# Kernel tuning notes

Hardware: AMD Instinct MI355X
Metric: run time of the kernel (lower is better)

## Reference

```python
import jax, jax.numpy as jnp
import numpy as np

NUM_TOKENS_SCORE = 64
NUM_HEADS = 16
NUM_KV_HEADS = 4
HEAD_SIZE = 128
SCALE = 0.08838834764831845  # 1/sqrt(128)


def setup_inputs() -> dict:
    key = jax.random.key(0)
    k1, k2, k3 = jax.random.split(key, 3)
    B, S = 2, 2048
    total = B * S
    return {
        "query": jax.random.normal(k1, (total, NUM_HEADS * HEAD_SIZE), dtype=jnp.float32),
        "key": jax.random.normal(k2, (total, NUM_KV_HEADS * HEAD_SIZE), dtype=jnp.float32),
        "value": jax.random.normal(k3, (total, NUM_KV_HEADS * HEAD_SIZE), dtype=jnp.float32),
        "batch_size": B,
        "seq_len": S,
    }


def reference(query, key, value, batch_size, seq_len):
    """Prompt-phase SparsePagedAttention: varlen causal GQA attention (equal
    prompt lengths -> dense [B,S] layout) plus the fused softmax score-sum over
    the last NUM_TOKENS_SCORE query rows used for KV-cache pruning."""
    B, S = batch_size, seq_len
    H, Hk, D = NUM_HEADS, NUM_KV_HEADS, HEAD_SIZE
    rep = H // Hk  # queries per kv head (head_mapping via repeat_interleave)

    q = query.reshape(B, S, H, D)
    k = jnp.repeat(key.reshape(B, S, Hk, D), rep, axis=2)    # [B,S,H,D]
    v = jnp.repeat(value.reshape(B, S, Hk, D), rep, axis=2)  # [B,S,H,D]

    scores = jnp.einsum('bqhd,bkhd->bhqk', q, k) * SCALE      # [B,H,S,S]
    causal = jnp.tril(jnp.ones((S, S), dtype=bool))
    scores = jnp.where(causal[None, None], scores, jnp.finfo(scores.dtype).min)
    probs = jax.nn.softmax(scores, axis=-1)                   # [B,H,S,S]

    out = jnp.einsum('bhqk,bkhd->bqhd', probs, v).reshape(B * S, H * D)
    # triton_fused_softmax_sum: sum softmax probs over last NUM_TOKENS_SCORE queries
    score_sum = probs[:, :, S - NUM_TOKENS_SCORE:, :].sum(axis=2)  # [B,H,S]
    return out, score_sum
```

## Files before the change

### kernel.cpp

```cpp
#include <hip/hip_runtime.h>


#define BB 2
#define SS 2048
#define NH 16
#define NKV 4
#define DD 128
#define TILE_SH 4096

typedef __attribute__((ext_vector_type(8))) short bf16x8;
typedef __attribute__((ext_vector_type(4))) float f32x4;

constexpr float SCL = 0.08838834764831845f * 1.4426950408889634f;

__device__ __forceinline__ short f2bf(float f) {
  union { float f; unsigned u; } v; v.f = f;
  unsigned r = v.u + 0x7FFFu + ((v.u >> 16) & 1u);
  return (short)(r >> 16);
}

__device__ __forceinline__ unsigned pack2bf(float a, float b) {
  union { float f; unsigned u; } x, y; x.f = a; y.f = b;
  return __builtin_amdgcn_perm(y.u, x.u, 0x07060302);
}

__device__ __forceinline__ void gl_lds16(const void* g, void* l) {
  __builtin_amdgcn_global_load_lds(
      (const __attribute__((address_space(1))) unsigned*)g,
      (__attribute__((address_space(3))) unsigned*)l, 16, 0, 0);
}

__global__ void prep(const float* __restrict__ K, const float* __restrict__ V,
                     short* __restrict__ Kb, short* __restrict__ Vb) {
  const int p = blockIdx.x;
  const int b = p >> 8, hk = (p >> 6) & 3, kt = p & 63;
  const int tid = threadIdx.x;
  const int k0 = kt * 32;
  short* kb = Kb + ((size_t)((b * 4 + hk) * 64 + kt)) * TILE_SH;
  short* vb = Vb + ((size_t)((b * 4 + hk) * 64 + kt)) * TILE_SH;
  {
    const int k = tid & 31, chb = tid >> 5;
    const float* src = K + ((size_t)(b * SS + k0 + k) * NKV + hk) * DD;
#pragma unroll
    for (int i = 0; i < 2; ++i) {
      const int ch = chb + i * 8;
      const float* s = src + ch * 8;
      float4 f0 = *(const float4*)s;
      float4 f1 = *(const float4*)(s + 4);
      bf16x8 t;
      t[0] = f2bf(f0.x); t[1] = f2bf(f0.y); t[2] = f2bf(f0.z); t[3] = f2bf(f0.w);
      t[4] = f2bf(f1.x); t[5] = f2bf(f1.y); t[6] = f2bf(f1.z); t[7] = f2bf(f1.w);
      *(bf16x8*)(kb + (ch * 32 + k) * 8) = t;
    }
  }
  {
    const int d = tid & 127, kcb = tid >> 7;
#pragma unroll
    for (int i = 0; i < 2; ++i) {
      const int kc = kcb + i * 2;
      const float* s = V + ((size_t)(b * SS + k0 + kc * 8) * NKV + hk) * DD + d;
      bf16x8 t;
#pragma unroll
      for (int e = 0; e < 8; ++e) t[e] = f2bf(s[(size_t)e * (NKV * DD)]);
      *(bf16x8*)(vb + (kc * 128 + d) * 8) = t;
    }
  }
}

__constant__ unsigned char RK2SLOT[48] = {
    15, 46, 47, 44, 45, 14, 42, 43, 40, 41, 13, 38, 39, 36, 37, 12,
    34, 35, 32, 33, 11, 30, 31, 28, 29, 10, 26, 27, 24, 25, 9,  22,
    23, 20, 21, 8,  18, 19, 16, 17, 7,  6,  5,  4,  3,  2,  1,  0};

__global__ __launch_bounds__(256, 4) void fa2(
    const float* __restrict__ Q, const short* __restrict__ Kb,
    const short* __restrict__ Vb, float* __restrict__ Out,
    float* __restrict__ Ob, float* __restrict__ l0a, float* __restrict__ l1a,
    float* __restrict__ wsl, const int mode) {
  __shared__ bf16x8 kv[2][1024];
  __shared__ short ldsP[4][640];

  const int tid = threadIdx.x;
  const int w = tid >> 6, lane = tid & 63;
  const int c = lane & 15, qd = lane >> 4;

  int qt, kb0, nit, part, bh;
  if (mode) {
    bh = blockIdx.x & 31;
    const int rank = blockIdx.x >> 5;
    const int slot = RK2SLOT[rank];
    if (slot < 16) {
      qt = slot; kb0 = 0; nit = 2 * qt + 2; part = 0;
    } else {
      const int s = slot - 16;
      qt = 16 + (s >> 1);
      if (s & 1) { kb0 = qt + 1; nit = qt + 1; part = 2; }
      else       { kb0 = 0;      nit = qt + 1; part = 1; }
    }
  } else {
    const int i = blockIdx.x;
    const int g = i >> 8, cc = i & 255;
    bh = cc >> 3;
    const int jp = cc & 7;
    qt = (g == 0) ? jp : (g == 1) ? 31 - jp : (g == 2) ? 8 + jp : 23 - jp;
    kb0 = 0; nit = 2 * qt + 2; part = 0;
  }
  const int b = bh >> 4, h = bh & 15, hk = h >> 2;

  const char* KT = (const char*)(Kb + ((size_t)(b * 4 + hk)) * 64 * TILE_SH);
  const char* VT = (const char*)(Vb + ((size_t)(b * 4 + hk)) * 64 * TILE_SH);

  auto stage = [&](int kt, int bi) {
    const char* sk = KT + (size_t)kt * 8192 + w * 2048 + lane * 16;
    const char* sv = VT + (size_t)kt * 8192 + w * 2048 + lane * 16;
    char* dk = (char*)kv[bi] + w * 2048;
    char* dv = dk + 8192;
#pragma unroll
    for (int t = 0; t < 2; ++t) {
      gl_lds16(sk + t * 1024, dk + t * 1024);
      gl_lds16(sv + t * 1024, dv + t * 1024);
    }
  };

  stage(kb0, 0);

  const float* qrow = Q + ((size_t)(b * SS + qt * 64 + w * 16 + c) * NH + h) * DD;
  bf16x8 qf[4];
#pragma unroll
  for (int ks = 0; ks < 4; ++ks) {
    const float* p = qrow + ks * 32 + qd * 8;
    float4 f0 = *(const float4*)p;
    float4 f1 = *(const float4*)(p + 4);
    bf16x8 t;
    t[0] = f2bf(f0.x * SCL); t[1] = f2bf(f0.y * SCL);
    t[2] = f2bf(f0.z * SCL); t[3] = f2bf(f0.w * SCL);
    t[4] = f2bf(f1.x * SCL); t[5] = f2bf(f1.y * SCL);
    t[6] = f2bf(f1.z * SCL); t[7] = f2bf(f1.w * SCL);
    qf[ks] = t;
  }

  f32x4 o[8];
#pragma unroll
  for (int dt = 0; dt < 8; ++dt) { o[dt][0] = 0.f; o[dt][1] = 0.f; o[dt][2] = 0.f; o[dt][3] = 0.f; }
  float l_part = 0.f;

  for (int it = 0; it < nit; ++it) {
    const int kt = kb0 + it;
    __syncthreads();
    const int cb = it & 1;
    if (it + 1 < nit) stage(kt + 1, cb ^ 1);

    const bf16x8* bK = kv[cb];
    const bf16x8* bV = kv[cb] + 512;

    f32x4 st0 = {0.f, 0.f, 0.f, 0.f}, st1 = {0.f, 0.f, 0.f, 0.f};
#pragma unroll
    for (int ks = 0; ks < 4; ++ks) {
      const int chz = (ks * 4 + qd) * 32;
      bf16x8 a0 = bK[chz + c];
      bf16x8 a1 = bK[chz + 16 + c];
      st0 = __builtin_amdgcn_mfma_f32_16x16x32_bf16(a0, qf[ks], st0, 0, 0, 0);
      st1 = __builtin_amdgcn_mfma_f32_16x16x32_bf16(a1, qf[ks], st1, 0, 0, 0);
    }

    float pr[8];
#pragma unroll
    for (int r = 0; r < 4; ++r) { pr[r] = exp2f(st0[r]); pr[4 + r] = exp2f(st1[r]); }
    const int koff = kt * 32 - qt * 64;
    if (koff >= 0) {
      const int qrl = w * 16 + c;
#pragma unroll
      for (int mt = 0; mt < 2; ++mt)
#pragma unroll
        for (int r = 0; r < 4; ++r)
          if (koff + mt * 16 + qd * 4 + r > qrl) pr[mt * 4 + r] = 0.f;
    }
#pragma unroll
    for (int x = 0; x < 8; ++x) l_part += pr[x];

    short* pp = ldsP[w] + c * 40;
#pragma unroll
    for (int mt = 0; mt < 2; ++mt) {
      union { short4 s4; unsigned u[2]; } pk;
      pk.u[0] = pack2bf(pr[mt * 4 + 0], pr[mt * 4 + 1]);
      pk.u[1] = pack2bf(pr[mt * 4 + 2], pr[mt * 4 + 3]);
      *(short4*)(pp + mt * 16 + qd * 4) = pk.s4;
    }
    __asm__ volatile("s_waitcnt lgkmcnt(0)" ::: "memory");
    bf16x8 pf = *(const bf16x8*)(pp + qd * 8);

#pragma unroll
    for (int dt = 0; dt < 8; ++dt)
      o[dt] = __builtin_amdgcn_mfma_f32_16x16x32_bf16(bV[qd * 128 + dt * 16 + c],
                                                      pf, o[dt], 0, 0, 0);
  }

  float l = l_part;
  l += __shfl_xor(l, 16);
  l += __shfl_xor(l, 32);

  if (part == 0) {
    const float linv = 1.f / l;
    float* orow = Out + ((size_t)(b * SS + qt * 64 + w * 16 + c) * NH + h) * DD;
#pragma unroll
    for (int dt = 0; dt < 8; ++dt) {
      float4 ov;
      ov.x = o[dt][0] * linv; ov.y = o[dt][1] * linv;
      ov.z = o[dt][2] * linv; ov.w = o[dt][3] * linv;
      *(float4*)(orow + dt * 16 + qd * 4) = ov;
    }
    if (!mode && qt == 31 && qd == 0)
      wsl[bh * 64 + w * 16 + c] = l;
  } else {
    const int qoff = (qt - 16) * 64 + w * 16 + c;
    float* dst = (part == 1)
        ? Out + ((size_t)(b * SS + qt * 64 + w * 16 + c) * NH + h) * DD
        : Ob + ((size_t)(bh * 1024 + qoff)) * DD;
#pragma unroll
    for (int dt = 0; dt < 8; ++dt)
      *(f32x4*)(dst + dt * 16 + qd * 4) = o[dt];
    if (qd == 0) {
      float* la = (part == 1) ? l0a : l1a;
      la[bh * 1024 + qoff] = l;
    }
  }
}

__global__ __launch_bounds__(256) void combine(
    float* __restrict__ Out, const float* __restrict__ Ob,
    const float* __restrict__ l0a, const float* __restrict__ l1a,
    float* __restrict__ wsl) {
  const int t = blockIdx.x * 256 + threadIdx.x;
  const int row = t >> 5;
  const int d4 = (t & 31) * 4;
  const int bh = row >> 10, qp = row & 1023;
  const int b = bh >> 4, h = bh & 15;
  const float lsum = l0a[row] + l1a[row];
  const float li = 1.f / lsum;
  float* po = Out + ((size_t)(b * SS + 1024 + qp) * NH + h) * DD + d4;
  const float4 a = *(const float4*)po;
  const float4 cc = *(const float4*)(Ob + (size_t)row * DD + d4);
  float4 r;
  r.x = (a.x + cc.x) * li; r.y = (a.y + cc.y) * li;
  r.z = (a.z + cc.z) * li; r.w = (a.w + cc.w) * li;
  *(float4*)po = r;
  if (qp >= 960 && (t & 31) == 0) wsl[bh * 64 + (qp - 960)] = lsum;
}

__global__ __launch_bounds__(256, 2) void score(
    const float* __restrict__ Q, const short* __restrict__ Kb,
    const float* __restrict__ wsl, float* __restrict__ out2) {
  __shared__ float ldsS[4][64];
  const int tid = threadIdx.x;
  const int w = tid >> 6, lane = tid & 63;
  const int c = lane & 15, qd = lane >> 4;
  const int bh = blockIdx.x & 31, kt = blockIdx.x >> 5;
  const int b = bh >> 4, h = bh & 15, hk = h >> 2;
  const int q0 = SS - 64;

  const float* qrow = Q + ((size_t)(b * SS + q0 + w * 16 + c) * NH + h) * DD;
  bf16x8 qf[4];
#pragma unroll
  for (int ks = 0; ks < 4; ++ks) {
    const float* p = qrow + ks * 32 + qd * 8;
    float4 f0 = *(const float4*)p;
    float4 f1 = *(const float4*)(p + 4);
    bf16x8 t;
    t[0] = f2bf(f0.x * SCL); t[1] = f2bf(f0.y * SCL);
    t[2] = f2bf(f0.z * SCL); t[3] = f2bf(f0.w * SCL);
    t[4] = f2bf(f1.x * SCL); t[5] = f2bf(f1.y * SCL);
    t[6] = f2bf(f1.z * SCL); t[7] = f2bf(f1.w * SCL);
    qf[ks] = t;
  }
  float linv[4];
  const int r0 = bh * 64 + w * 16 + qd * 4;
#pragma unroll
  for (int r = 0; r < 4; ++r) linv[r] = 1.f / wsl[r0 + r];

  const bf16x8* kb = (const bf16x8*)Kb + ((size_t)(b * 4 + hk) * 64 + kt * 2) * 512;
  f32x4 s[4];
#pragma unroll
  for (int nt = 0; nt < 4; ++nt) { s[nt][0] = 0.f; s[nt][1] = 0.f; s[nt][2] = 0.f; s[nt][3] = 0.f; }
#pragma unroll
  for (int ks = 0; ks < 4; ++ks) {
#pragma unroll
    for (int nt = 0; nt < 4; ++nt) {
      bf16x8 kf = kb[(nt >> 1) * 512 + (ks * 4 + qd) * 32 + (nt & 1) * 16 + c];
      s[nt] = __builtin_amdgcn_mfma_f32_16x16x32_bf16(qf[ks], kf, s[nt], 0, 0, 0);
    }
  }
  const bool diag = (kt == 31);
  float cs[4] = {0.f, 0.f, 0.f, 0.f};
#pragma unroll
  for (int nt = 0; nt < 4; ++nt) {
#pragma unroll
    for (int r = 0; r < 4; ++r) {
      float pv = exp2f(s[nt][r]) * linv[r];
      if (diag && nt * 16 + c > w * 16 + qd * 4 + r) pv = 0.f;
      cs[nt] += pv;
    }
    cs[nt] += __shfl_xor(cs[nt], 16);
    cs[nt] += __shfl_xor(cs[nt], 32);
  }
  if (lane < 16) {
#pragma unroll
    for (int nt = 0; nt < 4; ++nt) ldsS[w][nt * 16 + c] = cs[nt];
  }
  __syncthreads();
  if (tid < 64)
    out2[(size_t)bh * SS + kt * 64 + tid] =
        ldsS[0][tid] + ldsS[1][tid] + ldsS[2][tid] + ldsS[3][tid];
}

extern "C" void kernel_launch(void* const* d_in, const int* in_sizes, int n_in,
                              void* d_out, int out_size, void* d_ws, size_t ws_size,
                              hipStream_t stream) {
  const float* Q = (const float*)d_in[0];
  const float* K = (const float*)d_in[1];
  const float* V = (const float*)d_in[2];
  float* out = (float*)d_out;
  float* out2 = out + (size_t)BB * SS * NH * DD;

  short* Kb = (short*)d_ws;
  const size_t tsz = (size_t)2 * 4 * 64 * TILE_SH;
  short* Vb = Kb + tsz;
  float* aux = (float*)(Vb + tsz);

  float* Ob = aux;
  float* l0 = Ob + (size_t)32 * 1024 * 128;
  float* l1 = l0 + 32 * 1024;
  float* wsl_split = l1 + 32 * 1024;
  const size_t need = (size_t)((char*)(wsl_split + 32 * 64) - (char*)d_ws);
  const int mode = (ws_size >= need) ? 1 : 0;
  float* wsl = mode ? wsl_split : aux;

  hipLaunchKernelGGL(prep, dim3(512), dim3(256), 0, stream, K, V, Kb, Vb);
  hipLaunchKernelGGL(fa2, dim3(mode ? 1536 : 1024), dim3(256), 0, stream,
                     Q, Kb, Vb, out, Ob, l0, l1, wsl, mode);
  if (mode)
    hipLaunchKernelGGL(combine, dim3(4096), dim3(256), 0, stream,
                       out, Ob, l0, l1, wsl);
  hipLaunchKernelGGL(score, dim3(1024), dim3(256), 0, stream, Q, Kb, wsl, out2);
}
```

Measured before the change: 173.8 us.

## Load V fragments directly from global into registers and remap blocks to XCDs

V tiles are no longer staged through LDS. Each lane now reads its bf16 V fragments straight from global memory into registers at the start of each iteration, which halves the LDS footprint. With the smaller LDS use, the launch bound is raised from 4 to 6 blocks per CU. In mode 1 the block-index decode now places all heads sharing a KV head on the same XCD (blockIdx & 7) for L2 reuse, and the rank-to-slot ordering table is reshuffled. The risk is global-load latency on V that is not hidden by async staging, plus extra register pressure from holding eight V fragments.

After: 356.6 us. 105% more time.

```diff
diff --git a/kernel.cpp b/kernel.cpp
--- a/kernel.cpp
+++ b/kernel.cpp
@@ -68,27 +68,32 @@
 }
 
 __constant__ unsigned char RK2SLOT[48] = {
-    15, 46, 47, 44, 45, 14, 42, 43, 40, 41, 13, 38, 39, 36, 37, 12,
-    34, 35, 32, 33, 11, 30, 31, 28, 29, 10, 26, 27, 24, 25, 9,  22,
-    23, 20, 21, 8,  18, 19, 16, 17, 7,  6,  5,  4,  3,  2,  1,  0};
-
-__global__ __launch_bounds__(256, 4) void fa2(
+    15, 46, 47, 44, 45, 14, 42, 43,
+    40, 36, 13, 38, 39, 37, 41, 35,
+    12, 34, 32, 33, 30, 31, 10, 29,
+    28, 11, 26, 27, 24, 25, 22, 23,
+     9, 20, 21,  8, 18, 19, 16, 17,
+     0,  1,  2,  3,  4,  5,  6,  7};
+
+__global__ __launch_bounds__(256, 6) void fa2(
     const float* __restrict__ Q, const short* __restrict__ Kb,
     const short* __restrict__ Vb, float* __restrict__ Out,
     float* __restrict__ Ob, float* __restrict__ l0a, float* __restrict__ l1a,
     float* __restrict__ wsl, const int mode) {
-  __shared__ bf16x8 kv[2][1024];
+  __shared__ bf16x8 kv[2][512];
   __shared__ short ldsP[4][640];
 
   const int tid = threadIdx.x;
   const int w = tid >> 6, lane = tid & 63;
   const int c = lane & 15, qd = lane >> 4;
 
-  int qt, kb0, nit, part, bh;
+  int qt, kb0, nit, part, b, hk, h;
   if (mode) {
-    bh = blockIdx.x & 31;
-    const int rank = blockIdx.x >> 5;
+    const int xcd = blockIdx.x & 7;
+    const int r = blockIdx.x >> 3;
+    const int rank = r >> 2, hq = r & 3;
     const int slot = RK2SLOT[rank];
+    b = xcd >> 2; hk = xcd & 3; h = hk * 4 + hq;
     if (slot < 16) {
       qt = slot; kb0 = 0; nit = 2 * qt + 2; part = 0;
     } else {
@@ -100,26 +105,21 @@
   } else {
     const int i = blockIdx.x;
     const int g = i >> 8, cc = i & 255;
-    bh = cc >> 3;
-    const int jp = cc & 7;
+    const int bh0 = cc >> 3, jp = cc & 7;
     qt = (g == 0) ? jp : (g == 1) ? 31 - jp : (g == 2) ? 8 + jp : 23 - jp;
     kb0 = 0; nit = 2 * qt + 2; part = 0;
-  }
-  const int b = bh >> 4, h = bh & 15, hk = h >> 2;
+    b = bh0 >> 4; h = bh0 & 15; hk = h >> 2;
+  }
+  const int bh = b * 16 + h;
 
   const char* KT = (const char*)(Kb + ((size_t)(b * 4 + hk)) * 64 * TILE_SH);
   const char* VT = (const char*)(Vb + ((size_t)(b * 4 + hk)) * 64 * TILE_SH);
 
   auto stage = [&](int kt, int bi) {
     const char* sk = KT + (size_t)kt * 8192 + w * 2048 + lane * 16;
-    const char* sv = VT + (size_t)kt * 8192 + w * 2048 + lane * 16;
     char* dk = (char*)kv[bi] + w * 2048;
-    char* dv = dk + 8192;
-#pragma unroll
-    for (int t = 0; t < 2; ++t) {
-      gl_lds16(sk + t * 1024, dk + t * 1024);
-      gl_lds16(sv + t * 1024, dv + t * 1024);
-    }
+    gl_lds16(sk, dk);
+    gl_lds16(sk + 1024, dk + 1024);
   };
 
   stage(kb0, 0);
@@ -131,12 +131,12 @@
     const float* p = qrow + ks * 32 + qd * 8;
     float4 f0 = *(const float4*)p;
     float4 f1 = *(const float4*)(p + 4);
-    bf16x8 t;
-    t[0] = f2bf(f0.x * SCL); t[1] = f2bf(f0.y * SCL);
-    t[2] = f2bf(f0.z * SCL); t[3] = f2bf(f0.w * SCL);
-    t[4] = f2bf(f1.x * SCL); t[5] = f2bf(f1.y * SCL);
-    t[6] = f2bf(f1.z * SCL); t[7] = f2bf(f1.w * SCL);
-    qf[ks] = t;
+    bf16x8 tq;
+    tq[0] = f2bf(f0.x * SCL); tq[1] = f2bf(f0.y * SCL);
+    tq[2] = f2bf(f0.z * SCL); tq[3] = f2bf(f0.w * SCL);
+    tq[4] = f2bf(f1.x * SCL); tq[5] = f2bf(f1.y * SCL);
+    tq[6] = f2bf(f1.z * SCL); tq[7] = f2bf(f1.w * SCL);
+    qf[ks] = tq;
   }
 
   f32x4 o[8];
@@ -148,10 +148,15 @@
     const int kt = kb0 + it;
     __syncthreads();
     const int cb = it & 1;
+
+    bf16x8 av[8];
+    const bf16x8* vg = (const bf16x8*)(VT + (size_t)kt * 8192) + (qd * 128 + c);
+#pragma unroll
+    for (int dt = 0; dt < 8; ++dt) av[dt] = vg[dt * 16];
+
     if (it + 1 < nit) stage(kt + 1, cb ^ 1);
 
     const bf16x8* bK = kv[cb];
-    const bf16x8* bV = kv[cb] + 512;
 
     f32x4 st0 = {0.f, 0.f, 0.f, 0.f}, st1 = {0.f, 0.f, 0.f, 0.f};
 #pragma unroll
@@ -191,8 +196,7 @@
 
 #pragma unroll
     for (int dt = 0; dt < 8; ++dt)
-      o[dt] = __builtin_amdgcn_mfma_f32_16x16x32_bf16(bV[qd * 128 + dt * 16 + c],
-                                                      pf, o[dt], 0, 0, 0);
+      o[dt] = __builtin_amdgcn_mfma_f32_16x16x32_bf16(av[dt], pf, o[dt], 0, 0, 0);
   }
 
   float l = l_part;
```
